# Optimization experiments

Measured on AMD Instinct MI355X. Metric: run time of the kernel, lower is better.

The kernel has to match this reference:

```python
import jax, jax.numpy as jnp
import numpy as np

N, E, FN, FE, L, G = 4096, 16384, 16, 8, 128, 64
EPS = 1e-5


def setup_inputs() -> dict:
    key = jax.random.key(0)
    ks = iter(jax.random.split(key, 40))

    def lin_w(shape):
        return jax.random.normal(next(ks), shape, jnp.float32) * (1.0 / np.sqrt(shape[0]))

    d = {}
    d["x"] = jax.random.normal(next(ks), (N, FN), jnp.float32)
    d["edge_attr"] = jax.random.normal(next(ks), (E, FE), jnp.float32)
    d["edge_index"] = jax.random.randint(next(ks), (2, E), 0, N)
    d["batch"] = jnp.sort(jax.random.randint(next(ks), (N,), 0, G))
    for i, (cin, cout) in enumerate([(FN, 32), (32, 64), (64, 128)], 1):
        d[f"We{i}"] = lin_w((FE, cin * cout))          # edge_fc weight
        d[f"be{i}"] = jnp.zeros((cin * cout,), jnp.float32)
        d[f"bias{i}"] = jnp.zeros((cout,), jnp.float32)
        d[f"Wr{i}"] = lin_w((cin, cout))               # res_fc weight
        d[f"br{i}"] = jnp.zeros((cout,), jnp.float32)
        d[f"bn_g{i}"] = jnp.ones((cout,), jnp.float32)
        d[f"bn_b{i}"] = jnp.zeros((cout,), jnp.float32)
        d[f"a{i}"] = jnp.float32(0.25)                  # PReLU slope
    d["Wi"] = lin_w((128, 128)); d["bi"] = jnp.zeros((128,), jnp.float32)
    d["Wj"] = lin_w((128, 128)); d["bj"] = jnp.zeros((128,), jnp.float32)
    d["Wfc"] = lin_w((128, 2 * L)); d["bfc"] = jnp.zeros((2 * L,), jnp.float32)
    return d


def _ecc(x, src, dst, norm, edge_attr, We, be, bias, Wr, br, cout, cin):
    # dynamically generated per-edge filter: [E, out, in]
    theta = (edge_attr @ We + be).reshape(E, cout, cin)
    # gather source features, per-edge matvec, degree-normalize (norm_j)
    msg = norm[src][:, None] * jnp.einsum('eoi,ei->eo', theta, x[src])
    # scatter-add into destination nodes + bias + residual linear
    return jax.ops.segment_sum(msg, dst, num_segments=N) + bias + x @ Wr + br


def _bn(x, g, b):
    m = x.mean(0)
    v = x.var(0)  # biased variance, as torch BN training normalization
    return (x - m) * jax.lax.rsqrt(v + EPS) * g + b


def _prelu(x, a):
    return jnp.where(x >= 0, x, a * x)


def reference(x, edge_attr, edge_index, batch,
              We1, be1, bias1, Wr1, br1, bn_g1, bn_b1, a1,
              We2, be2, bias2, Wr2, br2, bn_g2, bn_b2, a2,
              We3, be3, bias3, Wr3, br3, bn_g3, bn_b3, a3,
              Wi, bi, Wj, bj, Wfc, bfc):
    src, dst = edge_index[0], edge_index[1]
    deg = jax.ops.segment_sum(jnp.ones((E,), x.dtype), src, num_segments=N)
    norm = jnp.where(deg > 0, 1.0 / deg, 0.0)

    h = _ecc(x, src, dst, norm, edge_attr, We1, be1, bias1, Wr1, br1, 32, FN)
    h = _prelu(_bn(h, bn_g1, bn_b1), a1)
    h = _ecc(h, src, dst, norm, edge_attr, We2, be2, bias2, Wr2, br2, 64, 32)
    h = _prelu(_bn(h, bn_g2, bn_b2), a2)
    h = _ecc(h, src, dst, norm, edge_attr, We3, be3, bias3, Wr3, br3, 128, 64)
    h = _prelu(_bn(h, bn_g3, bn_b3), a3)

    # gated attention pooling (GGS-NN eq. 7), scatter-sum per graph
    gates = jax.nn.sigmoid(h @ Wi + bi)
    feats = jnp.tanh(h @ Wj + bj)
    pooled = jnp.tanh(jax.ops.segment_sum(gates * feats, batch, num_segments=G))

    z = pooled @ Wfc + bfc  # [G, 2L]
    return z[:, :L], z[:, L:]
```

## Files before the change

kernel.cpp:

```cpp
#include <hip/hip_runtime.h>
#include <math.h>

#define NN 4096
#define NE 16384
#define NG 64

#define OFF_DEG   0
#define OFF_H1    4096
#define OFF_H2    135168
#define OFF_H3    397312
#define OFF_ST1   921600
#define OFF_ST2   921664
#define OFF_ST3   921792
#define OFF_POOL  922048
#define OFF_WC1   930240
#define OFF_WC2   934848
#define OFF_WC3   953280
#define OFF_Y     1027008
#define ZERO_FLOATS 930240

__device__ __forceinline__ void tr_wcat(const float* We, const float* be,
                                        float* Wcat, int CIN, int COUT, int t) {
    int nine = 9 * COUT;
    int i = t / nine; int r = t - i * nine;
    int f = r / COUT; int o = r - f * COUT;
    Wcat[t] = (f < 8) ? We[f * CIN * COUT + o * CIN + i] : be[o * CIN + i];
}

__global__ __launch_bounds__(256) void k_prep(
    const float* __restrict__ We1, const float* __restrict__ be1,
    const float* __restrict__ We2, const float* __restrict__ be2,
    const float* __restrict__ We3, const float* __restrict__ be3,
    const int* __restrict__ ei, float* __restrict__ ws)
{
    int t = blockIdx.x * 256 + threadIdx.x;
    if (t < 4608)  { tr_wcat(We1, be1, ws + OFF_WC1, 16, 32, t); return; }
    t -= 4608;
    if (t < 18432) { tr_wcat(We2, be2, ws + OFF_WC2, 32, 64, t); return; }
    t -= 18432;
    if (t < 73728) { tr_wcat(We3, be3, ws + OFF_WC3, 64, 128, t); return; }
    t -= 73728;
    if (t < NE)    { atomicAdd(&ws[OFF_DEG + ei[t]], 1.0f); }
}

template<int K, bool BN>
__global__ __launch_bounds__(256) void k_proj(
    const float* __restrict__ A,
    const float* __restrict__ B,
    const float* __restrict__ deg,
    float* __restrict__ Y, int Ncols,
    const float* __restrict__ st, const float* __restrict__ g,
    const float* __restrict__ b, const float* __restrict__ a)
{
    __shared__ float sA[K][68];
    __shared__ float sB[K][68];
    __shared__ float sS[K];
    __shared__ float sT[K];
    __shared__ float sAl;
    const int tid = threadIdx.x;
    const int m0 = blockIdx.x * 64;
    const int n0 = blockIdx.y * 64;

    if constexpr (BN) {
        if (tid < K) {
            float mean = st[tid] * (1.f / NN);
            float var  = st[K + tid] * (1.f / NN) - mean * mean;
            var = fmaxf(var, 0.f);
            float inv = rsqrtf(var + 1e-5f);
            float s = inv * g[tid];
            sS[tid] = s;
            sT[tid] = b[tid] - mean * s;
        }
        if (tid == 0) sAl = a[0];
    }
    __syncthreads();
    float al = 0.f;
    if constexpr (BN) al = sAl;

    for (int t = tid; t < 64 * K; t += 256) {
        int m = t / K, i = t - m * K;
        float v = A[(m0 + m) * K + i];
        if constexpr (BN) {
            v = fmaf(v, sS[i], sT[i]);
            v = v >= 0.f ? v : al * v;
        }
        sA[i][m] = v;
    }
    for (int t = tid; t < 64 * K; t += 256) {
        int i = t / 64, n = t - i * 64;
        int col = n0 + n;
        sB[i][n] = (col < Ncols) ? B[i * Ncols + col] : 0.f;
    }
    __syncthreads();

    const int tn = tid % 16, tm = tid / 16;
    float acc[4][4] = {{0.f}};
#pragma unroll 8
    for (int i = 0; i < K; ++i) {
        float4 av = *(const float4*)&sA[i][tm * 4];
        float4 bv = *(const float4*)&sB[i][tn * 4];
        acc[0][0] += av.x * bv.x; acc[0][1] += av.x * bv.y; acc[0][2] += av.x * bv.z; acc[0][3] += av.x * bv.w;
        acc[1][0] += av.y * bv.x; acc[1][1] += av.y * bv.y; acc[1][2] += av.y * bv.z; acc[1][3] += av.y * bv.w;
        acc[2][0] += av.z * bv.x; acc[2][1] += av.z * bv.y; acc[2][2] += av.z * bv.z; acc[2][3] += av.z * bv.w;
        acc[3][0] += av.w * bv.x; acc[3][1] += av.w * bv.y; acc[3][2] += av.w * bv.z; acc[3][3] += av.w * bv.w;
    }

#pragma unroll
    for (int mm = 0; mm < 4; ++mm) {
        int m = m0 + tm * 4 + mm;
        float d = deg[m];
        float nrm = d > 0.f ? 1.f / d : 0.f;
#pragma unroll
        for (int nn = 0; nn < 4; ++nn) {
            int col = n0 + tn * 4 + nn;
            if (col < Ncols) Y[(size_t)m * Ncols + col] = acc[mm][nn] * nrm;
        }
    }
}

template<int COUT>
__global__ __launch_bounds__(256) void k_egather(
    const float* __restrict__ Y, const float* __restrict__ eattr,
    const int* __restrict__ ei, float* __restrict__ h)
{
    constexpr int TPE = COUT / 4;
    int idx = blockIdx.x * 256 + threadIdx.x;
    int e = idx / TPE;
    int q = idx - e * TPE;
    int src = ei[e], dst = ei[NE + e];
    const float4* y4 = (const float4*)(Y + (size_t)src * (9 * COUT));
    const float4* ea4 = (const float4*)(eattr + e * 8);
    float4 ea0 = ea4[0], ea1 = ea4[1];
    float4 acc = y4[8 * TPE + q];
#define FMA4(s, v) { float4 _t = (v); acc.x += (s)*_t.x; acc.y += (s)*_t.y; acc.z += (s)*_t.z; acc.w += (s)*_t.w; }
    FMA4(ea0.x, y4[0 * TPE + q]);
    FMA4(ea0.y, y4[1 * TPE + q]);
    FMA4(ea0.z, y4[2 * TPE + q]);
    FMA4(ea0.w, y4[3 * TPE + q]);
    FMA4(ea1.x, y4[4 * TPE + q]);
    FMA4(ea1.y, y4[5 * TPE + q]);
    FMA4(ea1.z, y4[6 * TPE + q]);
    FMA4(ea1.w, y4[7 * TPE + q]);
#undef FMA4
    float* hp = h + (size_t)dst * COUT + 4 * q;
    atomicAdd(hp + 0, acc.x);
    atomicAdd(hp + 1, acc.y);
    atomicAdd(hp + 2, acc.z);
    atomicAdd(hp + 3, acc.w);
}

template<int CIN, int COUT, int KN, bool BN>
__global__ __launch_bounds__(256) void k_node(
    const float* __restrict__ xin, const float* __restrict__ Wr,
    const float* __restrict__ br, const float* __restrict__ bias,
    float* __restrict__ h, float* __restrict__ st_out,
    const float* __restrict__ st_in, const float* __restrict__ g,
    const float* __restrict__ b, const float* __restrict__ a)
{
    constexpr int NL = 256 / COUT;
    constexpr int NB = NL * KN;
    constexpr int CINP = CIN | 1;
    __shared__ float sWr[CIN * COUT];
    __shared__ float sX[NB * CINP];
    __shared__ float sred[256];
    __shared__ float sS[CIN];
    __shared__ float sT[CIN];
    __shared__ float sAl;
    const int tid = threadIdx.x;
    const int nbase = blockIdx.x * NB;

    if constexpr (BN) {
        if (tid < CIN) {
            float mean = st_in[tid] * (1.f / NN);
            float var  = st_in[CIN + tid] * (1.f / NN) - mean * mean;
            var = fmaxf(var, 0.f);
            float inv = rsqrtf(var + 1e-5f);
            float s = inv * g[tid];
            sS[tid] = s;
            sT[tid] = b[tid] - mean * s;
        }
        if (tid == 0) sAl = a[0];
    }
    for (int t = tid; t < CIN * COUT; t += 256) sWr[t] = Wr[t];
    __syncthreads();
    float al = 0.f;
    if constexpr (BN) al = sAl;

    for (int t = tid; t < NB * CIN; t += 256) {
        int r = t / CIN, i = t - r * CIN;
        float v = xin[(nbase + r) * CIN + i];
        if constexpr (BN) {
            v = fmaf(v, sS[i], sT[i]);
            v = v >= 0.f ? v : al * v;
        }
        sX[r * CINP + i] = v;
    }
    __syncthreads();

    const int o = tid % COUT;
    const int nl = tid / COUT;
    const float addc = bias[o] + br[o];
    float sum = 0.f, sumsq = 0.f;
    for (int k = 0; k < KN; ++k) {
        int r = nl * KN + k;
        float acc = addc;
        for (int i = 0; i < CIN; ++i)
            acc += sX[r * CINP + i] * sWr[i * COUT + o];
        int gi = (nbase + r) * COUT + o;
        float hv = h[gi] + acc;
        h[gi] = hv;
        sum += hv; sumsq += hv * hv;
    }
    sred[tid] = sum;
    __syncthreads();
    if (tid < COUT) {
        float s = 0.f;
        for (int g2 = 0; g2 < NL; ++g2) s += sred[g2 * COUT + tid];
        atomicAdd(&st_out[tid], s);
    }
    __syncthreads();
    sred[tid] = sumsq;
    __syncthreads();
    if (tid < COUT) {
        float s = 0.f;
        for (int g2 = 0; g2 < NL; ++g2) s += sred[g2 * COUT + tid];
        atomicAdd(&st_out[COUT + tid], s);
    }
}

__global__ __launch_bounds__(256) void k_pool(
    const float* __restrict__ h3, const int* __restrict__ batch,
    const float* __restrict__ Wi, const float* __restrict__ bi,
    const float* __restrict__ Wj, const float* __restrict__ bj,
    float* __restrict__ pooled,
    const float* __restrict__ st, const float* __restrict__ g,
    const float* __restrict__ b, const float* __restrict__ a)
{
    constexpr int KN = 8, NB = 16;
    __shared__ float sH[NB * 128];
    __shared__ int sB[NB];
    __shared__ float sS[128];
    __shared__ float sT[128];
    __shared__ float sAl;
    const int tid = threadIdx.x;
    const int nbase = blockIdx.x * NB;

    if (tid < 128) {
        float mean = st[tid] * (1.f / NN);
        float var  = st[128 + tid] * (1.f / NN) - mean * mean;
        var = fmaxf(var, 0.f);
        float inv = rsqrtf(var + 1e-5f);
        float s = inv * g[tid];
        sS[tid] = s;
        sT[tid] = b[tid] - mean * s;
    }
    if (tid == 0) sAl = a[0];
    __syncthreads();
    const float al = sAl;

    for (int t = tid; t < NB * 128; t += 256) {
        int c = t & 127;
        float v = h3[nbase * 128 + t];
        v = fmaf(v, sS[c], sT[c]);
        v = v >= 0.f ? v : al * v;
        sH[t] = v;
    }
    if (tid < NB) sB[tid] = batch[nbase + tid];
    __syncthreads();

    const int o = tid % 128, nl = tid / 128;
    float gacc[KN], facc[KN];
#pragma unroll
    for (int k = 0; k < KN; ++k) { gacc[k] = 0.f; facc[k] = 0.f; }
    for (int i = 0; i < 128; ++i) {
        float wi = Wi[i * 128 + o], wj = Wj[i * 128 + o];
#pragma unroll
        for (int k = 0; k < KN; ++k) {
            float hv = sH[(nl * KN + k) * 128 + i];
            gacc[k] += hv * wi;
            facc[k] += hv * wj;
        }
    }
    float bio = bi[o], bjo = bj[o];
#pragma unroll
    for (int k = 0; k < KN; ++k) {
        int r = nl * KN + k;
        float gate = 1.f / (1.f + expf(-(gacc[k] + bio)));
        float feat = tanhf(facc[k] + bjo);
        atomicAdd(&pooled[sB[r] * 128 + o], gate * feat);
    }
}

__global__ __launch_bounds__(256) void k_final(
    const float* __restrict__ pooled, const float* __restrict__ Wfc,
    const float* __restrict__ bfc, float* __restrict__ out)
{
    __shared__ float sP[128];
    const int g = blockIdx.x, c = threadIdx.x;
    if (c < 128) sP[c] = tanhf(pooled[g * 128 + c]);
    __syncthreads();
    float z = bfc[c];
    for (int i = 0; i < 128; ++i) z += sP[i] * Wfc[i * 256 + c];
    int oidx = (c < 128) ? (g * 128 + c) : (NG * 128 + g * 128 + (c - 128));
    out[oidx] = z;
}

extern "C" void kernel_launch(void* const* d_in, const int* in_sizes, int n_in,
                              void* d_out, int out_size, void* d_ws, size_t ws_size,
                              hipStream_t stream)
{
    (void)in_sizes; (void)n_in; (void)out_size; (void)ws_size;
    const float* x     = (const float*)d_in[0];
    const float* eattr = (const float*)d_in[1];
    const int*   ei    = (const int*)d_in[2];
    const int*   batch = (const int*)d_in[3];
    const float* We1 = (const float*)d_in[4];
    const float* be1 = (const float*)d_in[5];
    const float* bias1 = (const float*)d_in[6];
    const float* Wr1 = (const float*)d_in[7];
    const float* br1 = (const float*)d_in[8];
    const float* bg1 = (const float*)d_in[9];
    const float* bb1 = (const float*)d_in[10];
    const float* a1  = (const float*)d_in[11];
    const float* We2 = (const float*)d_in[12];
    const float* be2 = (const float*)d_in[13];
    const float* bias2 = (const float*)d_in[14];
    const float* Wr2 = (const float*)d_in[15];
    const float* br2 = (const float*)d_in[16];
    const float* bg2 = (const float*)d_in[17];
    const float* bb2 = (const float*)d_in[18];
    const float* a2  = (const float*)d_in[19];
    const float* We3 = (const float*)d_in[20];
    const float* be3 = (const float*)d_in[21];
    const float* bias3 = (const float*)d_in[22];
    const float* Wr3 = (const float*)d_in[23];
    const float* br3 = (const float*)d_in[24];
    const float* bg3 = (const float*)d_in[25];
    const float* bb3 = (const float*)d_in[26];
    const float* a3  = (const float*)d_in[27];
    const float* Wi  = (const float*)d_in[28];
    const float* bi  = (const float*)d_in[29];
    const float* Wj  = (const float*)d_in[30];
    const float* bj  = (const float*)d_in[31];
    const float* Wfc = (const float*)d_in[32];
    const float* bfc = (const float*)d_in[33];
    float* ws  = (float*)d_ws;
    float* out = (float*)d_out;

    hipMemsetAsync(d_ws, 0, (size_t)ZERO_FLOATS * sizeof(float), stream);
    k_prep<<<442, 256, 0, stream>>>(We1, be1, We2, be2, We3, be3, ei, ws);

    k_proj<16, false><<<dim3(64, 5), 256, 0, stream>>>(
        x, ws + OFF_WC1, ws + OFF_DEG, ws + OFF_Y, 288,
        nullptr, nullptr, nullptr, nullptr);
    k_egather<32><<<NE * 8 / 256, 256, 0, stream>>>(ws + OFF_Y, eattr, ei, ws + OFF_H1);
    k_node<16, 32, 2, false><<<NN / 16, 256, 0, stream>>>(
        x, Wr1, br1, bias1, ws + OFF_H1, ws + OFF_ST1,
        nullptr, nullptr, nullptr, nullptr);

    k_proj<32, true><<<dim3(64, 9), 256, 0, stream>>>(
        ws + OFF_H1, ws + OFF_WC2, ws + OFF_DEG, ws + OFF_Y, 576,
        ws + OFF_ST1, bg1, bb1, a1);
    k_egather<64><<<NE * 16 / 256, 256, 0, stream>>>(ws + OFF_Y, eattr, ei, ws + OFF_H2);
    k_node<32, 64, 4, true><<<NN / 16, 256, 0, stream>>>(
        ws + OFF_H1, Wr2, br2, bias2, ws + OFF_H2, ws + OFF_ST2,
        ws + OFF_ST1, bg1, bb1, a1);

    k_proj<64, true><<<dim3(64, 18), 256, 0, stream>>>(
        ws + OFF_H2, ws + OFF_WC3, ws + OFF_DEG, ws + OFF_Y, 1152,
        ws + OFF_ST2, bg2, bb2, a2);
    k_egather<128><<<NE * 32 / 256, 256, 0, stream>>>(ws + OFF_Y, eattr, ei, ws + OFF_H3);
    k_node<64, 128, 8, true><<<NN / 16, 256, 0, stream>>>(
        ws + OFF_H2, Wr3, br3, bias3, ws + OFF_H3, ws + OFF_ST3,
        ws + OFF_ST2, bg2, bb2, a2);

    k_pool<<<NN / 16, 256, 0, stream>>>(ws + OFF_H3, batch, Wi, bi, Wj, bj, ws + OFF_POOL,
                                        ws + OFF_ST3, bg3, bb3, a3);
    k_final<<<NG, 256, 0, stream>>>(ws + OFF_POOL, Wfc, bfc, out);
}
```

Measured before the change: 295.5 us.

## Fuse pooling with final FC via graph ranges; scalarize edge gather; retune node tiling

Computes per-graph node ranges from the sorted batch vector in the prep kernel. Pooling and the final linear layer are fused into one kernel with one block per graph, which removes the pooled atomics and one launch. The tradeoff is only 64 blocks of parallelism for the gate/feature matmuls. The edge gather also changes from float4 per thread to one scalar output per thread, with four times as many threads and scalar atomics, and the node kernels for layers 1 and 2 process more nodes per block.

After: 276.3 us. 6.5% less time.

```diff
diff --git a/kernel.cpp b/kernel.cpp
--- a/kernel.cpp
+++ b/kernel.cpp
@@ -17,6 +17,7 @@
 #define OFF_WC2   934848
 #define OFF_WC3   953280
 #define OFF_Y     1027008
+#define OFF_GR    5745600
 #define ZERO_FLOATS 930240
 
 __device__ __forceinline__ void tr_wcat(const float* We, const float* be,
@@ -31,7 +32,8 @@
     const float* __restrict__ We1, const float* __restrict__ be1,
     const float* __restrict__ We2, const float* __restrict__ be2,
     const float* __restrict__ We3, const float* __restrict__ be3,
-    const int* __restrict__ ei, float* __restrict__ ws)
+    const int* __restrict__ ei, const int* __restrict__ batch,
+    float* __restrict__ ws)
 {
     int t = blockIdx.x * 256 + threadIdx.x;
     if (t < 4608)  { tr_wcat(We1, be1, ws + OFF_WC1, 16, 32, t); return; }
@@ -40,15 +42,22 @@
     t -= 18432;
     if (t < 73728) { tr_wcat(We3, be3, ws + OFF_WC3, 64, 128, t); return; }
     t -= 73728;
-    if (t < NE)    { atomicAdd(&ws[OFF_DEG + ei[t]], 1.0f); }
+    if (t < NE)    { atomicAdd(&ws[OFF_DEG + ei[t]], 1.0f); return; }
+    t -= NE;
+    if (t < NN) {
+        int* gr = (int*)(ws + OFF_GR);
+        int b1 = batch[t];
+        int b0 = (t == 0) ? -1 : batch[t - 1];
+        for (int g = b0 + 1; g <= b1; ++g) gr[g] = t;
+        if (t == NN - 1)
+            for (int g = b1 + 1; g <= NG; ++g) gr[g] = NN;
+    }
 }
 
 template<int K, bool BN>
 __global__ __launch_bounds__(256) void k_proj(
-    const float* __restrict__ A,
-    const float* __restrict__ B,
-    const float* __restrict__ deg,
-    float* __restrict__ Y, int Ncols,
+    const float* __restrict__ A, const float* __restrict__ Bm,
+    const float* __restrict__ deg, float* __restrict__ Y, int Ncols,
     const float* __restrict__ st, const float* __restrict__ g,
     const float* __restrict__ b, const float* __restrict__ a)
 {
@@ -56,26 +65,23 @@
     __shared__ float sB[K][68];
     __shared__ float sS[K];
     __shared__ float sT[K];
-    __shared__ float sAl;
     const int tid = threadIdx.x;
     const int m0 = blockIdx.x * 64;
     const int n0 = blockIdx.y * 64;
 
+    float al = 0.f;
     if constexpr (BN) {
         if (tid < K) {
             float mean = st[tid] * (1.f / NN);
             float var  = st[K + tid] * (1.f / NN) - mean * mean;
             var = fmaxf(var, 0.f);
-            float inv = rsqrtf(var + 1e-5f);
-            float s = inv * g[tid];
+            float s = rsqrtf(var + 1e-5f) * g[tid];
             sS[tid] = s;
             sT[tid] = b[tid] - mean * s;
         }
-        if (tid == 0) sAl = a[0];
-    }
-    __syncthreads();
-    float al = 0.f;
-    if constexpr (BN) al = sAl;
+        al = a[0];
+        __syncthreads();
+    }
 
     for (int t = tid; t < 64 * K; t += 256) {
         int m = t / K, i = t - m * K;
@@ -87,13 +93,13 @@
         sA[i][m] = v;
     }
     for (int t = tid; t < 64 * K; t += 256) {
-        int i = t / 64, n = t - i * 64;
+        int i = t >> 6, n = t & 63;
         int col = n0 + n;
-        sB[i][n] = (col < Ncols) ? B[i * Ncols + col] : 0.f;
-    }
-    __syncthreads();
-
-    const int tn = tid % 16, tm = tid / 16;
+        sB[i][n] = (col < Ncols) ? Bm[i * Ncols + col] : 0.f;
+    }
+    __syncthreads();
+
+    const int tn = tid & 15, tm = tid >> 4;
     float acc[4][4] = {{0.f}};
 #pragma unroll 8
     for (int i = 0; i < K; ++i) {
@@ -123,30 +129,16 @@
     const float* __restrict__ Y, const float* __restrict__ eattr,
     const int* __restrict__ ei, float* __restrict__ h)
 {
-    constexpr int TPE = COUT / 4;
     int idx = blockIdx.x * 256 + threadIdx.x;
-    int e = idx / TPE;
-    int q = idx - e * TPE;
+    int e = idx / COUT;
+    int o = idx - e * COUT;
     int src = ei[e], dst = ei[NE + e];
-    const float4* y4 = (const float4*)(Y + (size_t)src * (9 * COUT));
-    const float4* ea4 = (const float4*)(eattr + e * 8);
-    float4 ea0 = ea4[0], ea1 = ea4[1];
-    float4 acc = y4[8 * TPE + q];
-#define FMA4(s, v) { float4 _t = (v); acc.x += (s)*_t.x; acc.y += (s)*_t.y; acc.z += (s)*_t.z; acc.w += (s)*_t.w; }
-    FMA4(ea0.x, y4[0 * TPE + q]);
-    FMA4(ea0.y, y4[1 * TPE + q]);
-    FMA4(ea0.z, y4[2 * TPE + q]);
-    FMA4(ea0.w, y4[3 * TPE + q]);
-    FMA4(ea1.x, y4[4 * TPE + q]);
-    FMA4(ea1.y, y4[5 * TPE + q]);
-    FMA4(ea1.z, y4[6 * TPE + q]);
-    FMA4(ea1.w, y4[7 * TPE + q]);
-#undef FMA4
-    float* hp = h + (size_t)dst * COUT + 4 * q;
-    atomicAdd(hp + 0, acc.x);
-    atomicAdd(hp + 1, acc.y);
-    atomicAdd(hp + 2, acc.z);
-    atomicAdd(hp + 3, acc.w);
+    const float* y = Y + (size_t)src * (9 * COUT);
+    const float* ea = eattr + e * 8;
+    float acc = y[8 * COUT + o];
+#pragma unroll
+    for (int f = 0; f < 8; ++f) acc += ea[f] * y[f * COUT + o];
+    atomicAdd(&h[dst * COUT + o], acc);
 }
 
 template<int CIN, int COUT, int KN, bool BN>
@@ -165,7 +157,6 @@
     __shared__ float sred[256];
     __shared__ float sS[CIN];
     __shared__ float sT[CIN];
-    __shared__ float sAl;
     const int tid = threadIdx.x;
     const int nbase = blockIdx.x * NB;
 
@@ -174,17 +165,15 @@
             float mean = st_in[tid] * (1.f / NN);
             float var  = st_in[CIN + tid] * (1.f / NN) - mean * mean;
             var = fmaxf(var, 0.f);
-            float inv = rsqrtf(var + 1e-5f);
-            float s = inv * g[tid];
+            float s = rsqrtf(var + 1e-5f) * g[tid];
             sS[tid] = s;
             sT[tid] = b[tid] - mean * s;
         }
-        if (tid == 0) sAl = a[0];
     }
     for (int t = tid; t < CIN * COUT; t += 256) sWr[t] = Wr[t];
     __syncthreads();
     float al = 0.f;
-    if constexpr (BN) al = sAl;
+    if constexpr (BN) al = a[0];
 
     for (int t = tid; t < NB * CIN; t += 256) {
         int r = t / CIN, i = t - r * CIN;
@@ -215,7 +204,7 @@
     __syncthreads();
     if (tid < COUT) {
         float s = 0.f;
-        for (int g2 = 0; g2 < NL; ++g2) s += sred[g2 * COUT + tid];
+        for (int q = 0; q < NL; ++q) s += sred[q * COUT + tid];
         atomicAdd(&st_out[tid], s);
     }
     __syncthreads();
@@ -223,85 +212,85 @@
     __syncthreads();
     if (tid < COUT) {
         float s = 0.f;
-        for (int g2 = 0; g2 < NL; ++g2) s += sred[g2 * COUT + tid];
+        for (int q = 0; q < NL; ++q) s += sred[q * COUT + tid];
         atomicAdd(&st_out[COUT + tid], s);
     }
 }
 
-__global__ __launch_bounds__(256) void k_pool(
-    const float* __restrict__ h3, const int* __restrict__ batch,
+__global__ __launch_bounds__(256) void k_poolfinal(
+    const float* __restrict__ h3, const float* __restrict__ gr_f,
     const float* __restrict__ Wi, const float* __restrict__ bi,
     const float* __restrict__ Wj, const float* __restrict__ bj,
-    float* __restrict__ pooled,
+    const float* __restrict__ Wfc, const float* __restrict__ bfc,
     const float* __restrict__ st, const float* __restrict__ g,
-    const float* __restrict__ b, const float* __restrict__ a)
-{
-    constexpr int KN = 8, NB = 16;
-    __shared__ float sH[NB * 128];
-    __shared__ int sB[NB];
+    const float* __restrict__ b, const float* __restrict__ a,
+    float* __restrict__ out)
+{
+    __shared__ float sH[16 * 128];
     __shared__ float sS[128];
     __shared__ float sT[128];
-    __shared__ float sAl;
+    __shared__ float sred[256];
+    __shared__ float sP[128];
     const int tid = threadIdx.x;
-    const int nbase = blockIdx.x * NB;
+    const int gid = blockIdx.x;
+    const int* gr = (const int*)gr_f;
+    const int r0 = gr[gid], r1 = gr[gid + 1];
 
     if (tid < 128) {
         float mean = st[tid] * (1.f / NN);
         float var  = st[128 + tid] * (1.f / NN) - mean * mean;
         var = fmaxf(var, 0.f);
-        float inv = rsqrtf(var + 1e-5f);
-        float s = inv * g[tid];
+        float s = rsqrtf(var + 1e-5f) * g[tid];
         sS[tid] = s;
         sT[tid] = b[tid] - mean * s;
     }
-    if (tid == 0) sAl = a[0];
-    __syncthreads();
-    const float al = sAl;
-
-    for (int t = tid; t < NB * 128; t += 256) {
-        int c = t & 127;
-        float v = h3[nbase * 128 + t];
-        v = fmaf(v, sS[c], sT[c]);
-        v = v >= 0.f ? v : al * v;
-        sH[t] = v;
-    }
-    if (tid < NB) sB[tid] = batch[nbase + tid];
-    __syncthreads();
-
-    const int o = tid % 128, nl = tid / 128;
-    float gacc[KN], facc[KN];
-#pragma unroll
-    for (int k = 0; k < KN; ++k) { gacc[k] = 0.f; facc[k] = 0.f; }
-    for (int i = 0; i < 128; ++i) {
-        float wi = Wi[i * 128 + o], wj = Wj[i * 128 + o];
-#pragma unroll
-        for (int k = 0; k < KN; ++k) {
-            float hv = sH[(nl * KN + k) * 128 + i];
-            gacc[k] += hv * wi;
-            facc[k] += hv * wj;
-        }
-    }
-    float bio = bi[o], bjo = bj[o];
-#pragma unroll
-    for (int k = 0; k < KN; ++k) {
-        int r = nl * KN + k;
-        float gate = 1.f / (1.f + expf(-(gacc[k] + bio)));
-        float feat = tanhf(facc[k] + bjo);
-        atomicAdd(&pooled[sB[r] * 128 + o], gate * feat);
-    }
-}
-
-__global__ __launch_bounds__(256) void k_final(
-    const float* __restrict__ pooled, const float* __restrict__ Wfc,
-    const float* __restrict__ bfc, float* __restrict__ out)
-{
-    __shared__ float sP[128];
-    const int g = blockIdx.x, c = threadIdx.x;
-    if (c < 128) sP[c] = tanhf(pooled[g * 128 + c]);
-    __syncthreads();
-    float z = bfc[c];
-    for (int i = 0; i < 128; ++i) z += sP[i] * Wfc[i * 256 + c];
-    int oidx = (c < 128) ? (g * 128 + c) : (NG * 128 + g * 128 + (c - 128));
+    __syncthreads();
+    const float al = a[0];
+    const int o = tid & 127, nl = tid >> 7;
+    const float bio = bi[o], bjo = bj[o];
+    float psum = 0.f;
+
+    for (int base = r0; base < r1; base += 16) {
+        __syncthreads();
+        int cnt = min(16, r1 - base);
+        for (int t = tid; t < cnt * 128; t += 256) {
+            int c = t & 127;
+            float v = h3[base * 128 + t];
+            v = fmaf(v, sS[c], sT[c]);
+            v = v >= 0.f ? v : al * v;
+            sH[t] = v;
+        }
+        __syncthreads();
+        float gacc[8], facc[8];
+#pragma unroll
+        for (int k = 0; k < 8; ++k) { gacc[k] = 0.f; facc[k] = 0.f; }
+        for (int i = 0; i < 128; ++i) {
+            float wi = Wi[i * 128 + o], wj = Wj[i * 128 + o];
+#pragma unroll
+            for (int k = 0; k < 8; ++k) {
+                float hv = sH[(nl * 8 + k) * 128 + i];
+                gacc[k] += hv * wi;
+                facc[k] += hv * wj;
+            }
+        }
+#pragma unroll
+        for (int k = 0; k < 8; ++k) {
+            int r = base + nl * 8 + k;
+            if (r < r1) {
+                float gate = 1.f / (1.f + expf(-(gacc[k] + bio)));
+                float feat = tanhf(facc[k] + bjo);
+                psum += gate * feat;
+            }
+        }
+    }
+
+    sred[tid] = psum;
+    __syncthreads();
+    if (tid < 128) sP[tid] = tanhf(sred[tid] + sred[128 + tid]);
+    __syncthreads();
+    float z = bfc[tid];
+    for (int i = 0; i < 128; ++i) z += sP[i] * Wfc[i * 256 + tid];
+    int oidx = (tid < 128) ? (gid * 128 + tid) : (NG * 128 + gid * 128 + (tid - 128));
     out[oidx] = z;
 }
 
@@ -348,33 +337,33 @@
     float* out = (float*)d_out;
 
     hipMemsetAsync(d_ws, 0, (size_t)ZERO_FLOATS * sizeof(float), stream);
-    k_prep<<<442, 256, 0, stream>>>(We1, be1, We2, be2, We3, be3, ei, ws);
+    k_prep<<<458, 256, 0, stream>>>(We1, be1, We2, be2, We3, be3, ei, batch, ws);
 
     k_proj<16, false><<<dim3(64, 5), 256, 0, stream>>>(
         x, ws + OFF_WC1, ws + OFF_DEG, ws + OFF_Y, 288,
         nullptr, nullptr, nullptr, nullptr);
-    k_egather<32><<<NE * 8 / 256, 256, 0, stream>>>(ws + OFF_Y, eattr, ei, ws + OFF_H1);
-    k_node<16, 32, 2, false><<<NN / 16, 256, 0, stream>>>(
+    k_egather<32><<<NE * 32 / 256, 256, 0, stream>>>(ws + OFF_Y, eattr, ei, ws + OFF_H1);
+    k_node<16, 32, 8, false><<<NN / 64, 256, 0, stream>>>(
         x, Wr1, br1, bias1, ws + OFF_H1, ws + OFF_ST1,
         nullptr, nullptr, nullptr, nullptr);
 
     k_proj<32, true><<<dim3(64, 9), 256, 0, stream>>>(
         ws + OFF_H1, ws + OFF_WC2, ws + OFF_DEG, ws + OFF_Y, 576,
         ws + OFF_ST1, bg1, bb1, a1);
-    k_egather<64><<<NE * 16 / 256, 256, 0, stream>>>(ws + OFF_Y, eattr, ei, ws + OFF_H2);
-    k_node<32, 64, 4, true><<<NN / 16, 256, 0, stream>>>(
+    k_egather<64><<<NE * 64 / 256, 256, 0, stream>>>(ws + OFF_Y, eattr, ei, ws + OFF_H2);
+    k_node<32, 64, 8, true><<<NN / 32, 256, 0, stream>>>(
         ws + OFF_H1, Wr2, br2, bias2, ws + OFF_H2, ws + OFF_ST2,
         ws + OFF_ST1, bg1, bb1, a1);
 
     k_proj<64, true><<<dim3(64, 18), 256, 0, stream>>>(
         ws + OFF_H2, ws + OFF_WC3, ws + OFF_DEG, ws + OFF_Y, 1152,
         ws + OFF_ST2, bg2, bb2, a2);
-    k_egather<128><<<NE * 32 / 256, 256, 0, stream>>>(ws + OFF_Y, eattr, ei, ws + OFF_H3);
+    k_egather<128><<<NE * 128 / 256, 256, 0, stream>>>(ws + OFF_Y, eattr, ei, ws + OFF_H3);
     k_node<64, 128, 8, true><<<NN / 16, 256, 0, stream>>>(
         ws + OFF_H2, Wr3, br3, bias3, ws + OFF_H3, ws + OFF_ST3,
         ws + OFF_ST2, bg2, bb2, a2);
 
-    k_pool<<<NN / 16, 256, 0, stream>>>(ws + OFF_H3, batch, Wi, bi, Wj, bj, ws + OFF_POOL,
-                                        ws + OFF_ST3, bg3, bb3, a3);
-    k_final<<<NG, 256, 0, stream>>>(ws + OFF_POOL, Wfc, bfc, out);
-}
+    k_poolfinal<<<NG, 256, 0, stream>>>(
+        ws + OFF_H3, ws + OFF_GR, Wi, bi, Wj, bj, Wfc, bfc,
+        ws + OFF_ST3, bg3, bb3, a3, out);
+}
```
